# Optimization experiments

Hardware: AMD Instinct MI355X
Metric: run time of the kernel (lower is better)

Reference implementation:

```python
import jax, jax.numpy as jnp
import numpy as np

S = 7          # side
B = 2          # boxes per cell
C = 20         # classes
L = S * S      # grid cells
NOOBJ = 0.5 * 1.0
OBJ   = 0.5 * 1.0
CLS   = 0.5 * 1.0
COORD = 0.5 * 5.0


def setup_inputs() -> dict:
    key = jax.random.key(0)
    k1, k2, k3 = jax.random.split(key, 3)
    n = 16384
    preds = jax.random.uniform(k1, (n, L * (C + 5 * B)), dtype=jnp.float32)
    labels = jax.random.uniform(k2, (n, L * (1 + C + 4)), dtype=jnp.float32)
    lab = labels.reshape(n, L, 1 + C + 4)
    obj_flag = (jax.random.uniform(k3, (n, L)) < 0.15).astype(jnp.float32)
    lab = lab.at[:, :, 0].set(obj_flag)
    labels = lab.reshape(n, -1)
    return {"preds": preds, "labels": labels}


def _iou(t, o):
    # t, o: [..., 4] boxes in (cx, cy, w, h); returns [...]
    left   = jnp.maximum(t[..., 0] - 0.5 * t[..., 2], o[..., 0] - 0.5 * o[..., 2])
    right  = jnp.minimum(t[..., 0] + 0.5 * t[..., 2], o[..., 0] + 0.5 * o[..., 2])
    top    = jnp.maximum(t[..., 1] - 0.5 * t[..., 3], o[..., 1] - 0.5 * o[..., 3])
    bottom = jnp.minimum(t[..., 1] + 0.5 * t[..., 3], o[..., 1] + 0.5 * o[..., 3])
    w = right - left
    h = bottom - top
    invalid = (w < 0) | (h < 0)
    inter = jnp.where(invalid, 0.0, w * h)
    union = t[..., 2] * t[..., 3] + o[..., 2] * o[..., 3] - inter
    return jnp.where(invalid, 0.0, inter / jnp.maximum(union, 1e-12))


def reference(preds, labels):
    n = preds.shape[0]
    pcls  = preds[:, : L * C].reshape(n, L, C)                       # [n,L,C]
    pconf = preds[:, L * C : L * C + L * B].reshape(n, L, B)          # [n,L,B]
    pbox  = preds[:, L * C + L * B :].reshape(n, L, B, 4)             # [n,L,B,4]

    lab  = labels.reshape(n, L, 1 + C + 4)
    obj  = lab[:, :, 0] != 0                                          # [n,L]
    tcls = lab[:, :, 1 : 1 + C]                                       # [n,L,C]
    tbox = lab[:, :, 1 + C :]                                         # [n,L,4] raw

    # --- best-box selection (on detached predictions, like .detach() in torch) ---
    o_raw = jax.lax.stop_gradient(pbox)
    o = jnp.concatenate([o_raw[..., :2] / S, o_raw[..., 2:] ** 2], axis=-1)      # [n,L,B,4]
    t = jnp.concatenate([tbox[..., :2] / S, tbox[..., 2:]], axis=-1)[:, :, None] # [n,L,1,4]
    t = jax.lax.stop_gradient(t)

    iou  = _iou(t, o)                                                 # [n,L,B]
    rmse = jnp.sqrt(jnp.sum((t - o) ** 2, axis=-1))                   # [n,L,B]
    max_iou = jnp.max(iou, axis=-1)
    # if any IoU>0 pick first argmax of IoU, else first argmin of RMSE (best_rmse init 20)
    best = jnp.where(max_iou > 0, jnp.argmax(iou, axis=-1), jnp.argmin(rmse, axis=-1))  # [n,L]
    best_iou = jnp.take_along_axis(iou, best[:, :, None], axis=-1)[..., 0]        # [n,L]

    onehot = jnp.arange(B) == best[:, :, None]                        # [n,L,B]
    mask_best = obj[:, :, None] & onehot

    # confidence delta: noobject everywhere, overwritten at best box of object cells
    conf_delta = jnp.where(mask_best,
                           OBJ * (best_iou[:, :, None] - pconf) ** 2,
                           NOOBJ * pconf ** 2)

    # class delta (object cells only)
    cls_delta = jnp.where(obj[:, :, None], CLS * (tcls - pcls) ** 2, 0.0)

    # coord delta at best box: raw truth x,y and sqrt(truth w,h) vs raw preds
    pbest = jnp.take_along_axis(pbox, best[:, :, None, None], axis=2)[:, :, 0]    # [n,L,4]
    ttarget = jnp.concatenate([tbox[..., :2], jnp.sqrt(tbox[..., 2:])], axis=-1)  # [n,L,4]
    coord_delta = jnp.where(obj[:, :, None], COORD * (ttarget - pbest) ** 2, 0.0)

    return jnp.nansum(conf_delta) + jnp.nansum(cls_delta) + jnp.nansum(coord_delta)
```

## Files before the change

### kernel.cpp

```cpp
#include <hip/hip_runtime.h>


#define L_CELLS 49
#define PRED_ROW 1470
#define LAB_ROW 1225
#define CONF_BASE 980
#define BOX_BASE 1078
#define W_NOOBJ 0.5f
#define W_OBJ 0.5f
#define W_CLS 0.5f
#define W_COORD 2.5f
#define INV_S (1.0f / 7.0f)

#define LAB_SLOTS 308
#define WAVE_SLOTS 310

typedef int __attribute__((address_space(1))) as1_int;
typedef int __attribute__((address_space(3))) as3_int;

__global__ __launch_bounds__(256, 6) void yolo_loss_kernel(
    const float* __restrict__ preds, const float* __restrict__ labels,
    float* __restrict__ ws) {
  __shared__ float4 st[4][WAVE_SLOTS];

  const int tid = threadIdx.x;
  const int w = tid >> 6;
  const int lane = tid & 63;
  const int s = blockIdx.x * 4 + w;
  float4* stw = st[w];
  float* stf = (float*)stw;

  const float* lrow = labels + (size_t)s * LAB_ROW;
  const float* rp = preds + (size_t)s * PRED_ROW;
  const bool act = lane < L_CELLS;

  float objf = 0.0f;
  if (act) objf = lrow[25 * lane];

  float2 cf = *(const float2*)(rp + CONF_BASE + 2 * lane);

  size_t g0 = (size_t)s * LAB_ROW;
  size_t ga = g0 & ~(size_t)3;
  int loff = (int)(g0 - ga);
#pragma unroll
  for (int r = 0; r < 5; ++r) {
    int i = lane + 64 * r;
    if (i < LAB_SLOTS)
      __builtin_amdgcn_global_load_lds((const as1_int*)(labels + ga + 4 * (size_t)i),
                                       (as3_int*)(stf + 256 * r), 16, 0, 0);
  }
  __builtin_amdgcn_sched_barrier(0);

  const bool objm = act && (objf != 0.0f);
  float2 pc[10];
  float2 bq[4];
  if (objm) {
#pragma unroll
    for (int k = 0; k < 10; ++k)
      pc[k] = *(const float2*)(rp + 20 * lane + 2 * k);
#pragma unroll
    for (int k = 0; k < 4; ++k)
      bq[k] = *(const float2*)(rp + BOX_BASE + 8 * lane + 2 * k);
  }

  asm volatile("s_waitcnt vmcnt(0)" ::: "memory");
  __builtin_amdgcn_sched_barrier(0);

  const float* lab = stf + loff;

  float acc = 0.0f;
  if (act) {
    const int l = lane;
    float noobj_term = W_NOOBJ * (cf.x * cf.x + cf.y * cf.y);
    if (objm) {
      float bx[8] = {bq[0].x, bq[0].y, bq[1].x, bq[1].y,
                     bq[2].x, bq[2].y, bq[3].x, bq[3].y};
      float tx = lab[25 * l + 21], ty = lab[25 * l + 22];
      float tw = lab[25 * l + 23], th = lab[25 * l + 24];
      float t0 = tx * INV_S, t1 = ty * INV_S, t2 = tw, t3 = th;

      float iou[2], rmse2[2];
#pragma unroll
      for (int b = 0; b < 2; ++b) {
        float o0 = bx[4 * b + 0] * INV_S;
        float o1 = bx[4 * b + 1] * INV_S;
        float o2 = bx[4 * b + 2] * bx[4 * b + 2];
        float o3 = bx[4 * b + 3] * bx[4 * b + 3];
        float left = fmaxf(t0 - 0.5f * t2, o0 - 0.5f * o2);
        float right = fminf(t0 + 0.5f * t2, o0 + 0.5f * o2);
        float top = fmaxf(t1 - 0.5f * t3, o1 - 0.5f * o3);
        float bot = fminf(t1 + 0.5f * t3, o1 + 0.5f * o3);
        float wd = right - left;
        float h = bot - top;
        bool invalid = (wd < 0.0f) || (h < 0.0f);
        float inter = invalid ? 0.0f : wd * h;
        float uni = t2 * t3 + o2 * o3 - inter;
        iou[b] = invalid ? 0.0f : inter / fmaxf(uni, 1e-12f);
        float d0 = t0 - o0, d1 = t1 - o1, d2 = t2 - o2, d3 = t3 - o3;
        rmse2[b] = d0 * d0 + d1 * d1 + d2 * d2 + d3 * d3;
      }

      float max_iou = fmaxf(iou[0], iou[1]);
      int best;
      if (max_iou > 0.0f)
        best = (iou[1] > iou[0]) ? 1 : 0;
      else
        best = (rmse2[1] < rmse2[0]) ? 1 : 0;
      float best_iou = iou[best];

      float cb = (best == 0) ? cf.x : cf.y;
      float co = (best == 0) ? cf.y : cf.x;
      float db = best_iou - cb;
      float obj_term = W_OBJ * db * db + W_NOOBJ * co * co;

      float clsacc = 0.0f;
#pragma unroll
      for (int k = 0; k < 10; ++k) {
        float d0 = lab[25 * l + 1 + 2 * k] - pc[k].x;
        float d1 = lab[25 * l + 2 + 2 * k] - pc[k].y;
        clsacc += d0 * d0 + d1 * d1;
      }
      obj_term += W_CLS * clsacc;

      float e0 = tx - bx[best * 4 + 0];
      float e1 = ty - bx[best * 4 + 1];
      float e2 = sqrtf(tw) - bx[best * 4 + 2];
      float e3 = sqrtf(th) - bx[best * 4 + 3];
      obj_term += W_COORD * (e0 * e0 + e1 * e1 + e2 * e2 + e3 * e3);

      acc = obj_term;
    } else {
      acc = noobj_term;
    }
  }

#pragma unroll
  for (int o = 32; o > 0; o >>= 1) acc += __shfl_down(acc, o);

  __shared__ float wsum[4];
  if (lane == 0) wsum[w] = acc;
  __syncthreads();
  if (tid == 0) ws[blockIdx.x] = wsum[0] + wsum[1] + wsum[2] + wsum[3];
}

__global__ __launch_bounds__(1024) void final_reduce_kernel(
    const float* __restrict__ ws, float* __restrict__ out, int m) {
  float acc = 0.0f;
  for (int i = threadIdx.x; i < m; i += 1024) acc += ws[i];
#pragma unroll
  for (int o = 32; o > 0; o >>= 1) acc += __shfl_down(acc, o);
  __shared__ float wsum[16];
  int wave = threadIdx.x >> 6;
  int lane = threadIdx.x & 63;
  if (lane == 0) wsum[wave] = acc;
  __syncthreads();
  if (threadIdx.x == 0) {
    float sum = 0.0f;
#pragma unroll
    for (int i = 0; i < 16; ++i) sum += wsum[i];
    out[0] = sum;
  }
}

extern "C" void kernel_launch(void* const* d_in, const int* in_sizes, int n_in,
                              void* d_out, int out_size, void* d_ws, size_t ws_size,
                              hipStream_t stream) {
  const float* preds = (const float*)d_in[0];
  const float* labels = (const float*)d_in[1];
  float* out = (float*)d_out;
  float* ws = (float*)d_ws;
  int n = in_sizes[0] / PRED_ROW;
  int blocks = n / 4;

  yolo_loss_kernel<<<blocks, 256, 0, stream>>>(preds, labels, ws);
  final_reduce_kernel<<<1, 1024, 0, stream>>>(ws, out, blocks);
}
```

Before: 186.2 us.

## Process eight samples per wave with double-buffered LDS label prefetch

Each wave now loops over 8 samples instead of one. The next sample's labels are prefetched into a second LDS buffer, along with its objectness and confidence values, while the current sample's predictions load, so latency is amortised across iterations. The block-level shared-memory reduction is dropped; each wave writes its own partial sum and the final reduce runs over more entries. The grid shrinks 8x and launch bounds drop to 2 blocks per CU, which lowers the number of waves available to hide latency. The s_waitcnt vmcnt(0) each iteration also waits on the prefetch, which limits the overlap.

Result: slower. 191.7 us (+3.0%).

```diff
diff --git a/kernel.cpp b/kernel.cpp
--- a/kernel.cpp
+++ b/kernel.cpp
@@ -14,133 +14,158 @@
 
 #define LAB_SLOTS 308
 #define WAVE_SLOTS 310
+#define K_SAMP 8
 
 typedef int __attribute__((address_space(1))) as1_int;
 typedef int __attribute__((address_space(3))) as3_int;
 
-__global__ __launch_bounds__(256, 6) void yolo_loss_kernel(
+__global__ __launch_bounds__(256, 2) void yolo_loss_kernel(
     const float* __restrict__ preds, const float* __restrict__ labels,
     float* __restrict__ ws) {
-  __shared__ float4 st[4][WAVE_SLOTS];
+  __shared__ float4 st[4][2][WAVE_SLOTS];
 
   const int tid = threadIdx.x;
   const int w = tid >> 6;
   const int lane = tid & 63;
-  const int s = blockIdx.x * 4 + w;
-  float4* stw = st[w];
-  float* stf = (float*)stw;
-
-  const float* lrow = labels + (size_t)s * LAB_ROW;
-  const float* rp = preds + (size_t)s * PRED_ROW;
+  const int wid = blockIdx.x * 4 + w;
   const bool act = lane < L_CELLS;
-
-  float objf = 0.0f;
-  if (act) objf = lrow[25 * lane];
-
-  float2 cf = *(const float2*)(rp + CONF_BASE + 2 * lane);
-
-  size_t g0 = (size_t)s * LAB_ROW;
-  size_t ga = g0 & ~(size_t)3;
-  int loff = (int)(g0 - ga);
-#pragma unroll
-  for (int r = 0; r < 5; ++r) {
-    int i = lane + 64 * r;
-    if (i < LAB_SLOTS)
-      __builtin_amdgcn_global_load_lds((const as1_int*)(labels + ga + 4 * (size_t)i),
-                                       (as3_int*)(stf + 256 * r), 16, 0, 0);
+  const int ll = (lane < L_CELLS) ? lane : (L_CELLS - 1);
+
+  float objf_v[2];
+  float2 cf_v[2];
+
+  {
+    const int s = wid * K_SAMP;
+    const float* lrow = labels + (size_t)s * LAB_ROW;
+    const float* rp = preds + (size_t)s * PRED_ROW;
+    objf_v[0] = lrow[25 * ll];
+    cf_v[0] = *(const float2*)(rp + CONF_BASE + 2 * lane);
+    float* dst = (float*)st[w][0];
+    size_t ga = ((size_t)s * LAB_ROW) & ~(size_t)3;
+#pragma unroll
+    for (int r = 0; r < 5; ++r) {
+      int i = lane + 64 * r;
+      if (i < LAB_SLOTS)
+        __builtin_amdgcn_global_load_lds(
+            (const as1_int*)(labels + ga + 4 * (size_t)i),
+            (as3_int*)(dst + 256 * r), 16, 0, 0);
+    }
   }
-  __builtin_amdgcn_sched_barrier(0);
-
-  const bool objm = act && (objf != 0.0f);
-  float2 pc[10];
-  float2 bq[4];
-  if (objm) {
-#pragma unroll
-    for (int k = 0; k < 10; ++k)
-      pc[k] = *(const float2*)(rp + 20 * lane + 2 * k);
-#pragma unroll
-    for (int k = 0; k < 4; ++k)
-      bq[k] = *(const float2*)(rp + BOX_BASE + 8 * lane + 2 * k);
+
+  float acc = 0.0f;
+
+#pragma unroll
+  for (int g = 0; g < K_SAMP; ++g) {
+    const int cur = g & 1;
+    const int s = wid * K_SAMP + g;
+    const float* rp = preds + (size_t)s * PRED_ROW;
+
+    const bool objm = act && (objf_v[cur] != 0.0f);
+
+    float2 pc[10];
+    float2 bq[4];
+    if (objm) {
+#pragma unroll
+      for (int k = 0; k < 10; ++k)
+        pc[k] = *(const float2*)(rp + 20 * lane + 2 * k);
+#pragma unroll
+      for (int k = 0; k < 4; ++k)
+        bq[k] = *(const float2*)(rp + BOX_BASE + 8 * lane + 2 * k);
+    }
+
+    if (g + 1 < K_SAMP) {
+      const int nxt = cur ^ 1;
+      const int sn = s + 1;
+      const float* lrown = labels + (size_t)sn * LAB_ROW;
+      const float* rpn = preds + (size_t)sn * PRED_ROW;
+      objf_v[nxt] = lrown[25 * ll];
+      cf_v[nxt] = *(const float2*)(rpn + CONF_BASE + 2 * lane);
+      float* dst = (float*)st[w][nxt];
+      size_t ga = ((size_t)sn * LAB_ROW) & ~(size_t)3;
+#pragma unroll
+      for (int r = 0; r < 5; ++r) {
+        int i = lane + 64 * r;
+        if (i < LAB_SLOTS)
+          __builtin_amdgcn_global_load_lds(
+              (const as1_int*)(labels + ga + 4 * (size_t)i),
+              (as3_int*)(dst + 256 * r), 16, 0, 0);
+      }
+    }
+
+    asm volatile("s_waitcnt vmcnt(0)" ::: "memory");
+    __builtin_amdgcn_sched_barrier(0);
+
+    const float* lab = (const float*)st[w][cur] + (g & 3);
+
+    if (act) {
+      const int l = lane;
+      float c0v = cf_v[cur].x, c1v = cf_v[cur].y;
+      if (objm) {
+        float bx[8] = {bq[0].x, bq[0].y, bq[1].x, bq[1].y,
+                       bq[2].x, bq[2].y, bq[3].x, bq[3].y};
+        float tx = lab[25 * l + 21], ty = lab[25 * l + 22];
+        float tw = lab[25 * l + 23], th = lab[25 * l + 24];
+        float t0 = tx * INV_S, t1 = ty * INV_S, t2 = tw, t3 = th;
+
+        float iou[2], rmse2[2];
+#pragma unroll
+        for (int b = 0; b < 2; ++b) {
+          float o0 = bx[4 * b + 0] * INV_S;
+          float o1 = bx[4 * b + 1] * INV_S;
+          float o2 = bx[4 * b + 2] * bx[4 * b + 2];
+          float o3 = bx[4 * b + 3] * bx[4 * b + 3];
+          float left = fmaxf(t0 - 0.5f * t2, o0 - 0.5f * o2);
+          float right = fminf(t0 + 0.5f * t2, o0 + 0.5f * o2);
+          float top = fmaxf(t1 - 0.5f * t3, o1 - 0.5f * o3);
+          float bot = fminf(t1 + 0.5f * t3, o1 + 0.5f * o3);
+          float wd = right - left;
+          float h = bot - top;
+          bool invalid = (wd < 0.0f) || (h < 0.0f);
+          float inter = invalid ? 0.0f : wd * h;
+          float uni = t2 * t3 + o2 * o3 - inter;
+          iou[b] = invalid ? 0.0f : inter / fmaxf(uni, 1e-12f);
+          float d0 = t0 - o0, d1 = t1 - o1, d2 = t2 - o2, d3 = t3 - o3;
+          rmse2[b] = d0 * d0 + d1 * d1 + d2 * d2 + d3 * d3;
+        }
+
+        float max_iou = fmaxf(iou[0], iou[1]);
+        int best;
+        if (max_iou > 0.0f)
+          best = (iou[1] > iou[0]) ? 1 : 0;
+        else
+          best = (rmse2[1] < rmse2[0]) ? 1 : 0;
+        float best_iou = iou[best];
+
+        float cb = (best == 0) ? c0v : c1v;
+        float co = (best == 0) ? c1v : c0v;
+        float db = best_iou - cb;
+        float obj_term = W_OBJ * db * db + W_NOOBJ * co * co;
+
+        float clsacc = 0.0f;
+#pragma unroll
+        for (int k = 0; k < 10; ++k) {
+          float d0 = lab[25 * l + 1 + 2 * k] - pc[k].x;
+          float d1 = lab[25 * l + 2 + 2 * k] - pc[k].y;
+          clsacc += d0 * d0 + d1 * d1;
+        }
+        obj_term += W_CLS * clsacc;
+
+        float e0 = tx - bx[best * 4 + 0];
+        float e1 = ty - bx[best * 4 + 1];
+        float e2 = sqrtf(tw) - bx[best * 4 + 2];
+        float e3 = sqrtf(th) - bx[best * 4 + 3];
+        obj_term += W_COORD * (e0 * e0 + e1 * e1 + e2 * e2 + e3 * e3);
+
+        acc += obj_term;
+      } else {
+        acc += W_NOOBJ * (c0v * c0v + c1v * c1v);
+      }
+    }
   }
 
-  asm volatile("s_waitcnt vmcnt(0)" ::: "memory");
-  __builtin_amdgcn_sched_barrier(0);
-
-  const float* lab = stf + loff;
-
-  float acc = 0.0f;
-  if (act) {
-    const int l = lane;
-    float noobj_term = W_NOOBJ * (cf.x * cf.x + cf.y * cf.y);
-    if (objm) {
-      float bx[8] = {bq[0].x, bq[0].y, bq[1].x, bq[1].y,
-                     bq[2].x, bq[2].y, bq[3].x, bq[3].y};
-      float tx = lab[25 * l + 21], ty = lab[25 * l + 22];
-      float tw = lab[25 * l + 23], th = lab[25 * l + 24];
-      float t0 = tx * INV_S, t1 = ty * INV_S, t2 = tw, t3 = th;
-
-      float iou[2], rmse2[2];
-#pragma unroll
-      for (int b = 0; b < 2; ++b) {
-        float o0 = bx[4 * b + 0] * INV_S;
-        float o1 = bx[4 * b + 1] * INV_S;
-        float o2 = bx[4 * b + 2] * bx[4 * b + 2];
-        float o3 = bx[4 * b + 3] * bx[4 * b + 3];
-        float left = fmaxf(t0 - 0.5f * t2, o0 - 0.5f * o2);
-        float right = fminf(t0 + 0.5f * t2, o0 + 0.5f * o2);
-        float top = fmaxf(t1 - 0.5f * t3, o1 - 0.5f * o3);
-        float bot = fminf(t1 + 0.5f * t3, o1 + 0.5f * o3);
-        float wd = right - left;
-        float h = bot - top;
-        bool invalid = (wd < 0.0f) || (h < 0.0f);
-        float inter = invalid ? 0.0f : wd * h;
-        float uni = t2 * t3 + o2 * o3 - inter;
-        iou[b] = invalid ? 0.0f : inter / fmaxf(uni, 1e-12f);
-        float d0 = t0 - o0, d1 = t1 - o1, d2 = t2 - o2, d3 = t3 - o3;
-        rmse2[b] = d0 * d0 + d1 * d1 + d2 * d2 + d3 * d3;
-      }
-
-      float max_iou = fmaxf(iou[0], iou[1]);
-      int best;
-      if (max_iou > 0.0f)
-        best = (iou[1] > iou[0]) ? 1 : 0;
-      else
-        best = (rmse2[1] < rmse2[0]) ? 1 : 0;
-      float best_iou = iou[best];
-
-      float cb = (best == 0) ? cf.x : cf.y;
-      float co = (best == 0) ? cf.y : cf.x;
-      float db = best_iou - cb;
-      float obj_term = W_OBJ * db * db + W_NOOBJ * co * co;
-
-      float clsacc = 0.0f;
-#pragma unroll
-      for (int k = 0; k < 10; ++k) {
-        float d0 = lab[25 * l + 1 + 2 * k] - pc[k].x;
-        float d1 = lab[25 * l + 2 + 2 * k] - pc[k].y;
-        clsacc += d0 * d0 + d1 * d1;
-      }
-      obj_term += W_CLS * clsacc;
-
-      float e0 = tx - bx[best * 4 + 0];
-      float e1 = ty - bx[best * 4 + 1];
-      float e2 = sqrtf(tw) - bx[best * 4 + 2];
-      float e3 = sqrtf(th) - bx[best * 4 + 3];
-      obj_term += W_COORD * (e0 * e0 + e1 * e1 + e2 * e2 + e3 * e3);
-
-      acc = obj_term;
-    } else {
-      acc = noobj_term;
-    }
-  }
-
 #pragma unroll
   for (int o = 32; o > 0; o >>= 1) acc += __shfl_down(acc, o);
-
-  __shared__ float wsum[4];
-  if (lane == 0) wsum[w] = acc;
-  __syncthreads();
-  if (tid == 0) ws[blockIdx.x] = wsum[0] + wsum[1] + wsum[2] + wsum[3];
+  if (lane == 0) ws[wid] = acc;
 }
 
 __global__ __launch_bounds__(1024) void final_reduce_kernel(
@@ -170,8 +195,9 @@
   float* out = (float*)d_out;
   float* ws = (float*)d_ws;
   int n = in_sizes[0] / PRED_ROW;
-  int blocks = n / 4;
+  int blocks = n / (4 * K_SAMP);
+  int nwaves = blocks * 4;
 
   yolo_loss_kernel<<<blocks, 256, 0, stream>>>(preds, labels, ws);
-  final_reduce_kernel<<<1, 1024, 0, stream>>>(ws, out, blocks);
+  final_reduce_kernel<<<1, 1024, 0, stream>>>(ws, out, nwaves);
 }
```
